# Kernel optimization log

Measured on AMD Instinct MI355X. Metric: run time of the kernel, lower is better.

The kernel has to match this reference:

```python
import jax, jax.numpy as jnp
import numpy as np

V = 128
L = 128
N = 4096

_ALPHA = "abcdefghijklmnopqrstuvwxyz"
TOKENS = (list("+-*/^()=") + [f"temp_{a}" for a in _ALPHA]
          + [str(d) for d in range(10)] + [f"w{i}" for i in range(84)])
assert len(TOKENS) == V
IDX = {t: i for i, t in enumerate(TOKENS)}
TEMPS = [f"temp_{a}" for a in _ALPHA]


def _build_mask_table() -> np.ndarray:
    """mask_table[p, v] = 0 if token v is illegal after prev-token p, else 1.
    Mirrors RuleFilter.single_filter's rho for every possible prev token."""
    M = np.ones((V, V), dtype=np.float32)

    def ban(prev_tokens, banned_tokens):
        cols = [IDX[t] for t in banned_tokens]
        for p in prev_tokens:
            M[IDX[p], cols] = 0.0

    ban(list("+-*/"), list("+-*/)="))          # prev is binary op
    ban(TEMPS, list("(="))                      # prev is temp_* variable
    ban(["="], list("+-*/=)") + TEMPS)         # prev is '='
    ban(["("], list("()+-*/="))                # prev is '('
    ban([")"], list("()") + TEMPS)             # prev is ')'
    ban(["^"], list("+-*/=)"))                 # prev is '^'
    return M


def setup_inputs() -> dict:
    key = jax.random.key(0)
    logits = jax.random.normal(key, (L, N, V), dtype=jnp.float32)
    mask_table = jnp.asarray(_build_mask_table())  # (V, V) rule lookup
    return {"logits": logits, "mask_table": mask_table}


def reference(logits, mask_table):
    """logits: (L, N, V); mask_table: (V, V). Sequential rule masking:
    logits[i] *= mask_table[argmax(filtered logits[i-1])]."""
    first = logits[0]  # row 0 is never filtered

    def step(carry, cur):
        # carry: previously *filtered* logits row (N, V)
        prev_idx = jnp.argmax(carry, axis=-1)          # (N,)
        new = cur * mask_table[prev_idx]               # gather + multiply
        return new, new

    _, rest = jax.lax.scan(step, first, logits[1:])
    return jnp.concatenate([first[None], rest], axis=0)
```

## Files before the change

kernel.cpp:

```cpp
#include <hip/hip_runtime.h>


constexpr int V = 128;
constexpr int L = 128;
constexpr int N = 4096;
constexpr int D  = 14;
constexpr int RD = D + 1;
constexpr unsigned ROWB = (unsigned)N * V * 4;

__device__ __forceinline__ float wave_max_dpp(float x) {
    int v = __float_as_int(x);
    const int ninf = __float_as_int(-__builtin_inff());
#define RF_STEP(ctrl)                                                          \
    {                                                                          \
        int s = __builtin_amdgcn_update_dpp(ninf, v, ctrl, 0xf, 0xf, false);   \
        v = __float_as_int(fmaxf(__int_as_float(v), __int_as_float(s)));       \
    }
    RF_STEP(0x111)
    RF_STEP(0x112)
    RF_STEP(0x114)
    RF_STEP(0x118)
    RF_STEP(0x142)
    RF_STEP(0x143)
#undef RF_STEP
    return __int_as_float(__builtin_amdgcn_readlane(v, 63));
}

__device__ __forceinline__ unsigned long long uniform_u64(const void* p) {
    unsigned long long x = (unsigned long long)p;
    unsigned lo = __builtin_amdgcn_readfirstlane((unsigned)x);
    unsigned hi = __builtin_amdgcn_readfirstlane((unsigned)(x >> 32));
    return ((unsigned long long)hi << 32) | lo;
}

template <int I>
struct Step {
    static __device__ __forceinline__ void run(float* ring, float* fbuf,
                                               const unsigned* tbl, int& prev,
                                               int hbase,
                                               unsigned long long lbase,
                                               unsigned long long obase,
                                               unsigned laneoff,
                                               unsigned xwa, unsigned xra) {
        constexpr int NW = ((L - 1 - I) < D ? (L - 1 - I) : D) + (I < D ? I : D);
        constexpr int rs = I % RD;

        if constexpr (I + D < L) {
            constexpr int ps = (I + D) % RD;
            unsigned voff = (unsigned)(I + D) * ROWB + laneoff;
            asm volatile("global_load_dword %0, %1, %2"
                         : "=&v"(ring[ps])
                         : "v"(voff), "s"(lbase));
        }

        asm volatile("s_waitcnt vmcnt(%c2)"
                     : "+v"(ring[rs])
                     : "v"(fbuf[rs]), "i"(NW));

        float c = ring[rs];
        float f;
        if constexpr (I == 0) {
            f = c;
        } else {
            unsigned t01  = (prev & 32) ? tbl[1] : tbl[0];
            unsigned t23  = (prev & 32) ? tbl[3] : tbl[2];
            unsigned word = (prev & 64) ? t23 : t01;
            unsigned bit  = (word >> (prev & 31)) & 1u;
            f = __int_as_float(__float_as_int(c) & (0u - bit));
        }
        fbuf[rs] = f;

        {
            unsigned voff = (unsigned)I * ROWB + laneoff;
            asm volatile("global_store_dword %0, %1, %2"
                         :
                         : "v"(voff), "v"(fbuf[rs]), "s"(obase));
        }

        if constexpr (I < L - 1) {
            float bv = wave_max_dpp(f);
            unsigned long long blt = __ballot(f == bv);
            int im = hbase + (__ffsll((unsigned long long)blt) - 1);

            unsigned long long pk =
                ((unsigned long long)(unsigned)im << 32) |
                (unsigned)__float_as_int(bv);
            constexpr int PAR = (I & 1) * 1024;
            asm volatile("ds_write_b64 %0, %1 offset:%c2"
                         :: "v"(xwa), "v"(pk), "i"(PAR));
            asm volatile("s_waitcnt lgkmcnt(0)");
            __builtin_amdgcn_s_barrier();
            unsigned long long got;
            asm volatile("ds_read_b64 %0, %1 offset:%c2"
                         : "=v"(got)
                         : "v"(xra), "i"(PAR));
            asm volatile("s_waitcnt lgkmcnt(0)" : "+v"(got));
            __builtin_amdgcn_sched_barrier(0);

            float bo = __int_as_float((int)(unsigned)(got & 0xFFFFFFFFull));
            int   io = (int)(got >> 32);
            bool take = (bo > bv) || ((bo == bv) && (io < im));
            prev = take ? io : im;
        }

        Step<I + 1>::run(ring, fbuf, tbl, prev, hbase, lbase, obase, laneoff,
                         xwa, xra);
    }
};
template <>
struct Step<L> {
    static __device__ __forceinline__ void run(float*, float*, const unsigned*,
                                               int&, int, unsigned long long,
                                               unsigned long long, unsigned,
                                               unsigned, unsigned) {}
};

__global__ __launch_bounds__(128, 8) void rule_filter_kernel(
    const float* __restrict__ logits,
    const float* __restrict__ mask_table,
    float* __restrict__ out)
{
    __shared__ unsigned long long xch[2][2][64];

    const int h    = threadIdx.x >> 6;
    const int lane = threadIdx.x & 63;
    const int n    = blockIdx.x;
    const int e    = h * 64 + lane;

    const unsigned long long lbase = uniform_u64(logits + (size_t)n * V);
    const unsigned long long obase = uniform_u64(out    + (size_t)n * V);
    const unsigned laneoff = (unsigned)e * 4;

    unsigned tbl[4];
#pragma unroll 1
    for (int w = 0; w < 4; ++w) {
        unsigned acc = 0;
#pragma unroll
        for (int b = 0; b < 32; ++b) {
            float m = mask_table[(size_t)(w * 32 + b) * V + e];
            acc |= (m != 0.0f ? 1u : 0u) << b;
        }
        tbl[w] = acc;
    }
    asm volatile("s_waitcnt vmcnt(0)" ::: "memory");

    float ring[RD];
    float fbuf[RD];
#pragma unroll
    for (int r = 0; r < RD; ++r) fbuf[r] = 0.0f;

#pragma unroll
    for (int r = 0; r < D; ++r) {
        unsigned voff = (unsigned)r * ROWB + laneoff;
        asm volatile("global_load_dword %0, %1, %2"
                     : "=&v"(ring[r])
                     : "v"(voff), "s"(lbase));
    }

    const unsigned xwa = (unsigned)(unsigned long long)&xch[0][h][lane];
    const unsigned xra = (unsigned)(unsigned long long)&xch[0][1 - h][lane];

    int prev = 0;
    Step<0>::run(ring, fbuf, tbl, prev, h * 64, lbase, obase, laneoff, xwa, xra);
}

extern "C" void kernel_launch(void* const* d_in, const int* in_sizes, int n_in,
                              void* d_out, int out_size, void* d_ws, size_t ws_size,
                              hipStream_t stream) {
    const float* logits     = (const float*)d_in[0];
    const float* mask_table = (const float*)d_in[1];
    float* out              = (float*)d_out;

    dim3 grid(N);
    dim3 block(128);
    rule_filter_kernel<<<grid, block, 0, stream>>>(logits, mask_table, out);
}
```

Before: 461.6 us.

## Restructure row pipeline into prologue/steady loop/epilogue with deeper prefetch and packed argmax

Replaces the fully unrolled 128-step template recursion with a prologue of 16 steps, a non-unrolled loop of six 16-step steady-state blocks, and a 16-step epilogue, with ring depth set to 16 so slot indices are power-of-two masks. Prefetch distance rises from 14 to 15 rows. The cross-wave argmax merge now encodes value (sign-flipped for ordering) and inverted index in one u64, so a single 64-bit max replaces the float compare plus tie-break logic. This aims to cut instruction-cache pressure and per-step ALU work, at the cost of loop overhead and extra ring registers.

```diff
diff --git a/kernel.cpp b/kernel.cpp
--- a/kernel.cpp
+++ b/kernel.cpp
@@ -4,9 +4,11 @@
 constexpr int V = 128;
 constexpr int L = 128;
 constexpr int N = 4096;
-constexpr int D  = 14;
-constexpr int RD = D + 1;
+constexpr int D  = 15;
+constexpr int RD = 16;
 constexpr unsigned ROWB = (unsigned)N * V * 4;
+
+typedef unsigned long long u64;
 
 __device__ __forceinline__ float wave_max_dpp(float x) {
     int v = __float_as_int(x);
@@ -16,103 +18,130 @@
         int s = __builtin_amdgcn_update_dpp(ninf, v, ctrl, 0xf, 0xf, false);   \
         v = __float_as_int(fmaxf(__int_as_float(v), __int_as_float(s)));       \
     }
-    RF_STEP(0x111)
-    RF_STEP(0x112)
-    RF_STEP(0x114)
-    RF_STEP(0x118)
-    RF_STEP(0x142)
-    RF_STEP(0x143)
+    RF_STEP(0x111) RF_STEP(0x112) RF_STEP(0x114) RF_STEP(0x118)
+    RF_STEP(0x142) RF_STEP(0x143)
 #undef RF_STEP
     return __int_as_float(__builtin_amdgcn_readlane(v, 63));
 }
 
-__device__ __forceinline__ unsigned long long uniform_u64(const void* p) {
-    unsigned long long x = (unsigned long long)p;
+__device__ __forceinline__ u64 uniform_u64(const void* p) {
+    u64 x = (u64)p;
     unsigned lo = __builtin_amdgcn_readfirstlane((unsigned)x);
     unsigned hi = __builtin_amdgcn_readfirstlane((unsigned)(x >> 32));
-    return ((unsigned long long)hi << 32) | lo;
-}
-
-template <int I>
-struct Step {
+    return ((u64)hi << 32) | lo;
+}
+
+template <int J, int NW, bool PF, bool FIRST, bool LAST>
+__device__ __forceinline__ void one_step(float* ring, float* fbuf,
+                                         const unsigned* tbl, int& prev,
+                                         unsigned ibase, u64 lbase, u64 obase,
+                                         unsigned xwa, unsigned xra, int hbase) {
+    constexpr int rs = J & 15;
+    constexpr int ps = (J + D) & 15;
+
+    if constexpr (PF) {
+        unsigned voff = ibase + (unsigned)(J + D) * ROWB;
+        asm volatile("global_load_dword %0, %1, %2"
+                     : "=&v"(ring[ps])
+                     : "v"(voff), "s"(lbase));
+    }
+
+    asm volatile("s_waitcnt vmcnt(%c2)"
+                 : "+v"(ring[rs])
+                 : "v"(fbuf[rs]), "i"(NW));
+
+    float c = ring[rs];
+    float f;
+    if constexpr (FIRST) {
+        f = c;
+    } else {
+        unsigned w01  = (prev & 32) ? tbl[1] : tbl[0];
+        unsigned w23  = (prev & 32) ? tbl[3] : tbl[2];
+        unsigned word = (prev & 64) ? w23 : w01;
+        unsigned bit  = (word >> (prev & 31)) & 1u;
+        f = __int_as_float(__float_as_int(c) & (0u - bit));
+    }
+    fbuf[rs] = f;
+
+    {
+        unsigned voff = ibase + (unsigned)J * ROWB;
+        asm volatile("global_store_dword %0, %1, %2"
+                     :: "v"(voff), "v"(fbuf[rs]), "s"(obase));
+    }
+
+    if constexpr (!LAST) {
+        float bv = wave_max_dpp(f);
+        u64 blt  = __ballot(f == bv);
+        int im   = hbase + (__ffsll(blt) - 1);
+        unsigned b  = (unsigned)__float_as_int(bv);
+        unsigned sb = b ^ ((unsigned)((int)b >> 31) | 0x80000000u);
+        u64 pk = ((u64)sb << 32) | (unsigned)(127 - im);
+
+        constexpr int PAR = (J & 1) * 1024;
+        asm volatile("ds_write_b64 %0, %1 offset:%c2"
+                     :: "v"(xwa), "v"(pk), "i"(PAR));
+        asm volatile("s_waitcnt lgkmcnt(0)");
+        __builtin_amdgcn_s_barrier();
+        u64 got;
+        asm volatile("ds_read_b64 %0, %1 offset:%c2"
+                     : "=v"(got) : "v"(xra), "i"(PAR));
+        asm volatile("s_waitcnt lgkmcnt(0)" : "+v"(got));
+        __builtin_amdgcn_sched_barrier(0);
+
+        u64 m = (got > pk) ? got : pk;
+        prev = 127 - (int)((unsigned)m & 0x7Fu);
+    }
+}
+
+template <int J>
+struct Pro {
     static __device__ __forceinline__ void run(float* ring, float* fbuf,
                                                const unsigned* tbl, int& prev,
-                                               int hbase,
-                                               unsigned long long lbase,
-                                               unsigned long long obase,
-                                               unsigned laneoff,
-                                               unsigned xwa, unsigned xra) {
-        constexpr int NW = ((L - 1 - I) < D ? (L - 1 - I) : D) + (I < D ? I : D);
-        constexpr int rs = I % RD;
-
-        if constexpr (I + D < L) {
-            constexpr int ps = (I + D) % RD;
-            unsigned voff = (unsigned)(I + D) * ROWB + laneoff;
-            asm volatile("global_load_dword %0, %1, %2"
-                         : "=&v"(ring[ps])
-                         : "v"(voff), "s"(lbase));
-        }
-
-        asm volatile("s_waitcnt vmcnt(%c2)"
-                     : "+v"(ring[rs])
-                     : "v"(fbuf[rs]), "i"(NW));
-
-        float c = ring[rs];
-        float f;
-        if constexpr (I == 0) {
-            f = c;
-        } else {
-            unsigned t01  = (prev & 32) ? tbl[1] : tbl[0];
-            unsigned t23  = (prev & 32) ? tbl[3] : tbl[2];
-            unsigned word = (prev & 64) ? t23 : t01;
-            unsigned bit  = (word >> (prev & 31)) & 1u;
-            f = __int_as_float(__float_as_int(c) & (0u - bit));
-        }
-        fbuf[rs] = f;
-
-        {
-            unsigned voff = (unsigned)I * ROWB + laneoff;
-            asm volatile("global_store_dword %0, %1, %2"
-                         :
-                         : "v"(voff), "v"(fbuf[rs]), "s"(obase));
-        }
-
-        if constexpr (I < L - 1) {
-            float bv = wave_max_dpp(f);
-            unsigned long long blt = __ballot(f == bv);
-            int im = hbase + (__ffsll((unsigned long long)blt) - 1);
-
-            unsigned long long pk =
-                ((unsigned long long)(unsigned)im << 32) |
-                (unsigned)__float_as_int(bv);
-            constexpr int PAR = (I & 1) * 1024;
-            asm volatile("ds_write_b64 %0, %1 offset:%c2"
-                         :: "v"(xwa), "v"(pk), "i"(PAR));
-            asm volatile("s_waitcnt lgkmcnt(0)");
-            __builtin_amdgcn_s_barrier();
-            unsigned long long got;
-            asm volatile("ds_read_b64 %0, %1 offset:%c2"
-                         : "=v"(got)
-                         : "v"(xra), "i"(PAR));
-            asm volatile("s_waitcnt lgkmcnt(0)" : "+v"(got));
-            __builtin_amdgcn_sched_barrier(0);
-
-            float bo = __int_as_float((int)(unsigned)(got & 0xFFFFFFFFull));
-            int   io = (int)(got >> 32);
-            bool take = (bo > bv) || ((bo == bv) && (io < im));
-            prev = take ? io : im;
-        }
-
-        Step<I + 1>::run(ring, fbuf, tbl, prev, hbase, lbase, obase, laneoff,
-                         xwa, xra);
-    }
-};
-template <>
-struct Step<L> {
+                                               unsigned ibase, u64 lb, u64 ob,
+                                               unsigned xwa, unsigned xra, int hb) {
+        one_step<J, D + J, true, (J == 0), false>(ring, fbuf, tbl, prev, ibase,
+                                                  lb, ob, xwa, xra, hb);
+        Pro<J + 1>::run(ring, fbuf, tbl, prev, ibase, lb, ob, xwa, xra, hb);
+    }
+};
+template <> struct Pro<16> {
     static __device__ __forceinline__ void run(float*, float*, const unsigned*,
-                                               int&, int, unsigned long long,
-                                               unsigned long long, unsigned,
-                                               unsigned, unsigned) {}
+                                               int&, unsigned, u64, u64,
+                                               unsigned, unsigned, int) {}
+};
+
+template <int J>
+struct Steady {
+    static __device__ __forceinline__ void run(float* ring, float* fbuf,
+                                               const unsigned* tbl, int& prev,
+                                               unsigned ibase, u64 lb, u64 ob,
+                                               unsigned xwa, unsigned xra, int hb) {
+        one_step<J, 2 * D, true, false, false>(ring, fbuf, tbl, prev, ibase,
+                                               lb, ob, xwa, xra, hb);
+        Steady<J + 1>::run(ring, fbuf, tbl, prev, ibase, lb, ob, xwa, xra, hb);
+    }
+};
+template <> struct Steady<16> {
+    static __device__ __forceinline__ void run(float*, float*, const unsigned*,
+                                               int&, unsigned, u64, u64,
+                                               unsigned, unsigned, int) {}
+};
+
+template <int J>
+struct Epi {
+    static __device__ __forceinline__ void run(float* ring, float* fbuf,
+                                               const unsigned* tbl, int& prev,
+                                               unsigned ibase, u64 lb, u64 ob,
+                                               unsigned xwa, unsigned xra, int hb) {
+        one_step<J, (J == 0 ? 2 * D : 2 * D - J), (J == 0), false, (J == 15)>(
+            ring, fbuf, tbl, prev, ibase, lb, ob, xwa, xra, hb);
+        Epi<J + 1>::run(ring, fbuf, tbl, prev, ibase, lb, ob, xwa, xra, hb);
+    }
+};
+template <> struct Epi<16> {
+    static __device__ __forceinline__ void run(float*, float*, const unsigned*,
+                                               int&, unsigned, u64, u64,
+                                               unsigned, unsigned, int) {}
 };
 
 __global__ __launch_bounds__(128, 8) void rule_filter_kernel(
@@ -120,15 +149,15 @@
     const float* __restrict__ mask_table,
     float* __restrict__ out)
 {
-    __shared__ unsigned long long xch[2][2][64];
+    __shared__ u64 xch[2][2][64];
 
     const int h    = threadIdx.x >> 6;
     const int lane = threadIdx.x & 63;
     const int n    = blockIdx.x;
     const int e    = h * 64 + lane;
 
-    const unsigned long long lbase = uniform_u64(logits + (size_t)n * V);
-    const unsigned long long obase = uniform_u64(out    + (size_t)n * V);
+    const u64 lbase = uniform_u64(logits + (size_t)n * V);
+    const u64 obase = uniform_u64(out    + (size_t)n * V);
     const unsigned laneoff = (unsigned)e * 4;
 
     unsigned tbl[4];
@@ -157,11 +186,25 @@
                      : "v"(voff), "s"(lbase));
     }
 
-    const unsigned xwa = (unsigned)(unsigned long long)&xch[0][h][lane];
-    const unsigned xra = (unsigned)(unsigned long long)&xch[0][1 - h][lane];
+    const unsigned xwa = (unsigned)(size_t)&xch[0][h][lane];
+    const unsigned xra = (unsigned)(size_t)&xch[0][1 - h][lane];
+    const int hbase = h * 64;
 
     int prev = 0;
-    Step<0>::run(ring, fbuf, tbl, prev, h * 64, lbase, obase, laneoff, xwa, xra);
+    unsigned ibase = laneoff;
+
+    Pro<0>::run(ring, fbuf, tbl, prev, ibase, lbase, obase, xwa, xra, hbase);
+    ibase += 16u * ROWB;
+
+#pragma unroll 1
+    for (int mm = 1; mm <= 6; ++mm) {
+        Steady<0>::run(ring, fbuf, tbl, prev, ibase, lbase, obase, xwa, xra, hbase);
+        ibase += 16u * ROWB;
+    }
+
+    Epi<0>::run(ring, fbuf, tbl, prev, ibase, lbase, obase, xwa, xra, hbase);
+
+    asm volatile("s_waitcnt vmcnt(0)" ::: "memory");
 }
 
 extern "C" void kernel_launch(void* const* d_in, const int* in_sizes, int n_in,
```

Measured after the change: 461.9 us. Within noise of the previous version (+0.1%).
